# Performance work log

Hardware: AMD Instinct MI355X
Metric: run time of the kernel (lower is better)

## Reference

```python
import jax, jax.numpy as jnp
import numpy as np

NA, NKPT, NC = 3, 17, 1
NO_DET = NC + 5              # 6
NO = NO_DET + 3 * NKPT       # 57
ANCHORS = np.array([[19,27,44,40,38,94],[96,68,86,152,180,137],[140,301,303,264,238,542]], dtype=np.float32).reshape(3, 3, 2)
STRIDES = np.array([8.0, 16.0, 32.0], dtype=np.float32)
CH = (256, 512, 1024)
HW = (80, 40, 20)
B = 16


def setup_inputs():
    key = jax.random.key(0)
    ks = jax.random.split(key, 18)
    d = {}
    ki = 0
    for i, (c, hw) in enumerate(zip(CH, HW)):
        d[f"f{i}"] = jax.random.normal(ks[ki], (B, c, hw, hw), jnp.float32); ki += 1
        d[f"ia{i}"] = jax.random.normal(ks[ki], (1, c, 1, 1), jnp.float32) * 0.02; ki += 1
        d[f"w{i}"] = jax.random.normal(ks[ki], (NA * NO_DET, c), jnp.float32) * (1.0 / np.sqrt(c)); ki += 1
        d[f"b{i}"] = jnp.zeros((NA * NO_DET,), jnp.float32)
        d[f"im{i}"] = 1.0 + jax.random.normal(ks[ki], (1, NA * NO_DET, 1, 1), jnp.float32) * 0.02; ki += 1
        d[f"wk{i}"] = jax.random.normal(ks[ki], (NA * 3 * NKPT, c), jnp.float32) * (1.0 / np.sqrt(c)); ki += 1
        d[f"bk{i}"] = jnp.zeros((NA * 3 * NKPT,), jnp.float32)
    return d


def _decode(feat, ia, w, b, im, wk, bk, anchors_l, stride):
    # ImplicitA -> 1x1 conv -> ImplicitM (det branch); plain 1x1 conv (kpt branch)
    det = jnp.einsum('bchw,oc->bohw', feat + ia, w) + b[None, :, None, None]
    det = det * im
    kpt = jnp.einsum('bchw,oc->bohw', feat, wk) + bk[None, :, None, None]
    x = jnp.concatenate([det, kpt], axis=1)          # (B, na*no, H, W)
    Bb, _, H, W = x.shape
    x = x.reshape(Bb, NA, NO, H, W).transpose(0, 1, 3, 4, 2)  # (B, na, H, W, no)
    yv, xv = jnp.meshgrid(jnp.arange(H), jnp.arange(W), indexing='ij')
    grid = jnp.stack([xv, yv], -1).astype(x.dtype)[None, None]  # (1,1,H,W,2)
    xd = jax.nn.sigmoid(x[..., :NO_DET])
    xy = (xd[..., 0:2] * 2.0 - 0.5 + grid) * stride
    wh = (xd[..., 2:4] * 2.0) ** 2 * anchors_l.reshape(1, NA, 1, 1, 2)
    kp = x[..., NO_DET:]                              # (B, na, H, W, 51)
    kx = (kp[..., 0::3] * 2.0 - 0.5 + grid[..., 0:1]) * stride
    ky = (kp[..., 1::3] * 2.0 - 0.5 + grid[..., 1:2]) * stride
    kc = jax.nn.sigmoid(kp[..., 2::3])
    kdec = jnp.stack([kx, ky, kc], -1).reshape(Bb, NA, H, W, 3 * NKPT)
    y = jnp.concatenate([xy, wh, xd[..., 4:], kdec], -1)  # (B, na, H, W, 57)
    return y.reshape(Bb, -1, NO)


def reference(f0, ia0, w0, b0, im0, wk0, bk0,
              f1, ia1, w1, b1, im1, wk1, bk1,
              f2, ia2, w2, b2, im2, wk2, bk2):
    anchors = jnp.asarray(ANCHORS)
    z0 = _decode(f0, ia0, w0, b0, im0, wk0, bk0, anchors[0], STRIDES[0])
    z1 = _decode(f1, ia1, w1, b1, im1, wk1, bk1, anchors[1], STRIDES[1])
    z2 = _decode(f2, ia2, w2, b2, im2, wk2, bk2, anchors[2], STRIDES[2])
    return jnp.concatenate([z0, z1, z2], axis=1)      # (B, 25200, 57)
```

## Files before the change

### kernel.cpp

```cpp
#include <hip/hip_runtime.h>
#include <hip/hip_bf16.h>

typedef __attribute__((ext_vector_type(8))) short short8;
typedef __attribute__((ext_vector_type(4))) float floatx4;

__device__ __forceinline__ float sigm(float x) { return 1.0f / (1.0f + __expf(-x)); }

__device__ __forceinline__ unsigned short f2bf(float v) {
  union { __hip_bfloat16 h; unsigned short u; } cv;
  cv.h = __float2bfloat16(v);
  return cv.u;
}

__device__ __forceinline__ void glds16(const void* g, void* l) {
  __builtin_amdgcn_global_load_lds((const __attribute__((address_space(1))) void*)g,
                                   (__attribute__((address_space(3))) void*)l, 16, 0, 0);
}

struct PrepArgs {
  const float *w, *b, *im, *ia, *wk, *bk;
  unsigned short* Wp;
  float* bias;
  int C;
};

__global__ void prep_kernel(PrepArgs A0, PrepArgs A1, PrepArgs A2) {
  PrepArgs A = (blockIdx.y == 0) ? A0 : (blockIdx.y == 1) ? A1 : A2;
  const int n = blockIdx.x;
  const int t = threadIdx.x;
  const int C = A.C;
  unsigned short* wrow = A.Wp + (size_t)n * C;
  if (n >= 171) {
    for (int k = t; k < C; k += 64) wrow[k] = 0;
    if (t == 0) A.bias[n] = 0.0f;
    return;
  }
  if (n < 18) {
    const float* src = A.w + (size_t)n * C;
    const float sc = A.im[n];
    float dot = 0.0f;
    for (int k = t; k < C; k += 64) {
      float v = src[k];
      dot += v * A.ia[k];
      wrow[k] = f2bf(v * sc);
    }
#pragma unroll
    for (int off = 32; off > 0; off >>= 1) dot += __shfl_down(dot, off);
    if (t == 0) A.bias[n] = sc * (A.b[n] + dot);
  } else {
    const float* src = A.wk + (size_t)(n - 18) * C;
    for (int k = t; k < C; k += 64) wrow[k] = f2bf(src[k]);
    if (t == 0) A.bias[n] = A.bk[n - 18];
  }
}

#define LDS_BYTES 34560

template <int SC, int C, int HW, int W>
__device__ __forceinline__ void gemm_decode(const float* __restrict__ feat,
                                            const unsigned short* __restrict__ Wp,
                                            const float* __restrict__ bias,
                                            float* __restrict__ out, int tile, char* smem) {
  constexpr float STRD = (SC == 0) ? 8.0f : (SC == 1) ? 16.0f : 32.0f;
  constexpr int ZOFF = (SC == 0) ? 0 : (SC == 1) ? 19200 : 24000;
  constexpr int I = C / 64;

  const int t = threadIdx.x;
  const int lane = t & 63;
  const int wv = t >> 6;
  const int l15 = lane & 15;
  const int quad = lane >> 4;

  unsigned short* Alds = (unsigned short*)smem;
  char* BB = smem + 9216;
  float* Elds = (float*)smem;

  const int mA = tile * 64 + lane;
  const int bA = mA / HW;
  const int pA = mA - bA * HW;
  const float* fbase = feat + ((size_t)bA * C + wv * 16) * (size_t)HW + pA;

  const int rsub = lane >> 3;
  const int csw = (lane & 7) ^ rsub;
  const char* WpB = (const char*)Wp;

  floatx4 acc[11];
#pragma unroll
  for (int nj = 0; nj < 11; ++nj) acc[nj] = (floatx4){0.f, 0.f, 0.f, 0.f};

  const unsigned short* aRd = Alds + (wv * 16 + l15) * 72 + quad * 8;
  const int c0 = quad ^ (l15 & 7);
  const char* bRd0 = BB + (size_t)l15 * 128 + c0 * 16;
  const char* bRd1 = BB + (size_t)l15 * 128 + (c0 ^ 4) * 16;

  float v[16];
  auto loadA = [&](int it) {
    const float* g = fbase + (size_t)it * 64 * HW;
#pragma unroll
    for (int kk = 0; kk < 16; ++kk) v[kk] = g[(size_t)kk * HW];
  };
  auto writeA = [&]() {
    short8 s0, s1;
#pragma unroll
    for (int j = 0; j < 8; ++j) {
      s0[j] = (short)f2bf(v[j]);
      s1[j] = (short)f2bf(v[j + 8]);
    }
    *(short8*)(Alds + lane * 72 + wv * 16) = s0;
    *(short8*)(Alds + lane * 72 + wv * 16 + 8) = s1;
  };

  loadA(0);
  for (int it = 0; it < I; ++it) {
    asm volatile("s_barrier" ::: "memory");
#pragma unroll
    for (int j = 0; j < 6; ++j) {
      const int rowb = wv * 48 + j * 8;
      const void* gsrc = WpB + ((size_t)(rowb + rsub) * C + (size_t)it * 64) * 2 + csw * 16;
      glds16(gsrc, BB + rowb * 128);
    }
    __builtin_amdgcn_sched_barrier(0);
    writeA();
    loadA((it + 1 < I) ? it + 1 : it);
    __builtin_amdgcn_sched_barrier(0);
    asm volatile("s_waitcnt vmcnt(16) lgkmcnt(0)\n\ts_barrier" ::: "memory");
    short8 af0 = *(const short8*)(aRd);
    short8 af1 = *(const short8*)(aRd + 32);
#pragma unroll
    for (int nj = 0; nj < 11; ++nj) {
      short8 b0 = *(const short8*)(bRd0 + (size_t)nj * 2048);
      short8 b1 = *(const short8*)(bRd1 + (size_t)nj * 2048);
      acc[nj] = __builtin_amdgcn_mfma_f32_16x16x32_bf16(af0, b0, acc[nj], 0, 0, 0);
      acc[nj] = __builtin_amdgcn_mfma_f32_16x16x32_bf16(af1, b1, acc[nj], 0, 0, 0);
    }
  }

  float bj[11];
#pragma unroll
  for (int nj = 0; nj < 11; ++nj) bj[nj] = bias[nj * 16 + l15];

#pragma unroll
  for (int c = 0; c < 2; ++c) {
    __syncthreads();
    if ((wv >> 1) == c) {
      const int rbase = (wv & 1) * 16 + quad * 4;
#pragma unroll
      for (int nj = 0; nj < 11; ++nj)
#pragma unroll
        for (int r = 0; r < 4; ++r)
          Elds[(rbase + r) * 180 + nj * 16 + l15] = acc[nj][r] + bj[nj];
    }
    __syncthreads();
    if (t < 192) {
      const int task = t >> 1, half = t & 1;
      const int row = task & 31, a = task >> 5;
      const int m = tile * 64 + c * 32 + row;
      const int bb = m / HW;
      const int p = m - bb * HW;
      const float fx = (float)(p % W);
      const float fy = (float)(p / W);
      float* L = Elds + row * 180 + a * 57;
      if (half == 0) {
        float aw, ah;
        if constexpr (SC == 0) {
          aw = (a == 0) ? 19.f : (a == 1) ? 44.f : 38.f;
          ah = (a == 0) ? 27.f : (a == 1) ? 40.f : 94.f;
        } else if constexpr (SC == 1) {
          aw = (a == 0) ? 96.f : (a == 1) ? 86.f : 180.f;
          ah = (a == 0) ? 68.f : (a == 1) ? 152.f : 137.f;
        } else {
          aw = (a == 0) ? 140.f : (a == 1) ? 303.f : 238.f;
          ah = (a == 0) ? 301.f : (a == 1) ? 264.f : 542.f;
        }
        float r0 = L[0], r1 = L[1], r2 = L[2], r3 = L[3], r4 = L[4], r5 = L[5];
        L[0] = (sigm(r0) * 2.f - 0.5f + fx) * STRD;
        L[1] = (sigm(r1) * 2.f - 0.5f + fy) * STRD;
        float tw = sigm(r2) * 2.f;
        L[2] = tw * tw * aw;
        float th = sigm(r3) * 2.f;
        L[3] = th * th * ah;
        L[4] = sigm(r4);
        L[5] = sigm(r5);
#pragma unroll
        for (int kp = 0; kp < 8; ++kp) {
          float kx = L[6 + 3 * kp], ky = L[7 + 3 * kp], kc = L[8 + 3 * kp];
          L[6 + 3 * kp] = (kx * 2.f - 0.5f + fx) * STRD;
          L[7 + 3 * kp] = (ky * 2.f - 0.5f + fy) * STRD;
          L[8 + 3 * kp] = sigm(kc);
        }
      } else {
#pragma unroll
        for (int kp = 8; kp < 17; ++kp) {
          float kx = L[6 + 3 * kp], ky = L[7 + 3 * kp], kc = L[8 + 3 * kp];
          L[6 + 3 * kp] = (kx * 2.f - 0.5f + fx) * STRD;
          L[7 + 3 * kp] = (ky * 2.f - 0.5f + fy) * STRD;
          L[8 + 3 * kp] = sigm(kc);
        }
      }
    }
    __syncthreads();
    for (int i = t; i < 96 * 57; i += 256) {
      int sr = i / 57;
      int j = i - sr * 57;
      int a = sr >> 5, row = sr & 31;
      int m = tile * 64 + c * 32 + row;
      int bb = m / HW;
      int p = m - bb * HW;
      out[((size_t)bb * 25200 + (size_t)(ZOFF + a * HW + p)) * 57 + j] =
          Elds[row * 180 + a * 57 + j];
    }
  }
}

__global__ __launch_bounds__(256, 4) void main_kernel(
    const float* __restrict__ f0, const float* __restrict__ f1, const float* __restrict__ f2,
    const unsigned short* __restrict__ Wp0, const unsigned short* __restrict__ Wp1,
    const unsigned short* __restrict__ Wp2, const float* __restrict__ b0,
    const float* __restrict__ b1, const float* __restrict__ b2, float* __restrict__ out) {
  __shared__ __align__(16) char smem[LDS_BYTES];
  const int bid = blockIdx.x;
  if (bid < 100)
    gemm_decode<2, 1024, 400, 20>(f2, Wp2, b2, out, bid, smem);
  else if (bid < 500)
    gemm_decode<1, 512, 1600, 40>(f1, Wp1, b1, out, bid - 100, smem);
  else
    gemm_decode<0, 256, 6400, 80>(f0, Wp0, b0, out, bid - 500, smem);
}

extern "C" void kernel_launch(void* const* d_in, const int* in_sizes, int n_in, void* d_out,
                              int out_size, void* d_ws, size_t ws_size, hipStream_t stream) {
  const float *f[3], *ia[3], *w[3], *b[3], *im[3], *wk[3], *bk[3];
  for (int s = 0; s < 3; ++s) {
    f[s] = (const float*)d_in[7 * s + 0];
    ia[s] = (const float*)d_in[7 * s + 1];
    w[s] = (const float*)d_in[7 * s + 2];
    b[s] = (const float*)d_in[7 * s + 3];
    im[s] = (const float*)d_in[7 * s + 4];
    wk[s] = (const float*)d_in[7 * s + 5];
    bk[s] = (const float*)d_in[7 * s + 6];
  }
  char* ws = (char*)d_ws;
  unsigned short* Wp0 = (unsigned short*)(ws + 0);
  unsigned short* Wp1 = (unsigned short*)(ws + 98304);
  unsigned short* Wp2 = (unsigned short*)(ws + 294912);
  float* bias0 = (float*)(ws + 688128);
  float* bias1 = (float*)(ws + 688896);
  float* bias2 = (float*)(ws + 689664);

  PrepArgs A0 = {w[0], b[0], im[0], ia[0], wk[0], bk[0], Wp0, bias0, 256};
  PrepArgs A1 = {w[1], b[1], im[1], ia[1], wk[1], bk[1], Wp1, bias1, 512};
  PrepArgs A2 = {w[2], b[2], im[2], ia[2], wk[2], bk[2], Wp2, bias2, 1024};
  prep_kernel<<<dim3(192, 3), 64, 0, stream>>>(A0, A1, A2);

  main_kernel<<<2100, 256, 0, stream>>>(f[0], f[1], f[2], Wp0, Wp1, Wp2, bias0, bias1, bias2,
                                        (float*)d_out);
}
```

Before: 298.9 us.

## Load A fragments directly into registers and double-buffer weight tiles in LDS

Each lane now loads the A operand straight from global memory in the MFMA fragment layout, converts it to bf16 in registers, and no longer round-trips it through LDS. That removes the LDS write/read of A and one barrier per K-iteration. The weight (B) tile is double-buffered in LDS so the next iteration's global-to-LDS copy overlaps the current MFMAs. The cost is more LDS per block (48KB), so the launch bound drops from 4 to 3 blocks per CU, and the per-lane global loads on feat may be less coalesced.

Result: no change. 296.9 us (-0.6%).

```diff
diff --git a/kernel.cpp b/kernel.cpp
--- a/kernel.cpp
+++ b/kernel.cpp
@@ -54,7 +54,7 @@
   }
 }
 
-#define LDS_BYTES 34560
+#define LDS_BYTES 49152
 
 template <int SC, int C, int HW, int W>
 __device__ __forceinline__ void gemm_decode(const float* __restrict__ feat,
@@ -71,14 +71,13 @@
   const int l15 = lane & 15;
   const int quad = lane >> 4;
 
-  unsigned short* Alds = (unsigned short*)smem;
-  char* BB = smem + 9216;
+  char* BB = smem;
   float* Elds = (float*)smem;
 
-  const int mA = tile * 64 + lane;
+  const int mA = tile * 64 + wv * 16 + l15;
   const int bA = mA / HW;
   const int pA = mA - bA * HW;
-  const float* fbase = feat + ((size_t)bA * C + wv * 16) * (size_t)HW + pA;
+  const float* fbase = feat + ((size_t)bA * C + quad * 8) * (size_t)HW + pA;
 
   const int rsub = lane >> 3;
   const int csw = (lane & 7) ^ rsub;
@@ -88,48 +87,49 @@
 #pragma unroll
   for (int nj = 0; nj < 11; ++nj) acc[nj] = (floatx4){0.f, 0.f, 0.f, 0.f};
 
-  const unsigned short* aRd = Alds + (wv * 16 + l15) * 72 + quad * 8;
   const int c0 = quad ^ (l15 & 7);
-  const char* bRd0 = BB + (size_t)l15 * 128 + c0 * 16;
-  const char* bRd1 = BB + (size_t)l15 * 128 + (c0 ^ 4) * 16;
+  const int bOff0 = l15 * 128 + c0 * 16;
+  const int bOff1 = l15 * 128 + (c0 ^ 4) * 16;
 
   float v[16];
   auto loadA = [&](int it) {
     const float* g = fbase + (size_t)it * 64 * HW;
 #pragma unroll
-    for (int kk = 0; kk < 16; ++kk) v[kk] = g[(size_t)kk * HW];
+    for (int j = 0; j < 8; ++j) {
+      v[j] = g[(size_t)j * HW];
+      v[j + 8] = g[(size_t)(32 + j) * HW];
+    }
   };
-  auto writeA = [&]() {
-    short8 s0, s1;
-#pragma unroll
-    for (int j = 0; j < 8; ++j) {
-      s0[j] = (short)f2bf(v[j]);
-      s1[j] = (short)f2bf(v[j + 8]);
-    }
-    *(short8*)(Alds + lane * 72 + wv * 16) = s0;
-    *(short8*)(Alds + lane * 72 + wv * 16 + 8) = s1;
-  };
-
-  loadA(0);
-  for (int it = 0; it < I; ++it) {
-    asm volatile("s_barrier" ::: "memory");
+  auto stageB = [&](int it, int buf) {
 #pragma unroll
     for (int j = 0; j < 6; ++j) {
       const int rowb = wv * 48 + j * 8;
       const void* gsrc = WpB + ((size_t)(rowb + rsub) * C + (size_t)it * 64) * 2 + csw * 16;
-      glds16(gsrc, BB + rowb * 128);
-    }
+      glds16(gsrc, BB + buf * 24576 + rowb * 128);
+    }
+  };
+
+  stageB(0, 0);
+  loadA(0);
+
+  for (int it = 0; it < I; ++it) {
+    asm volatile("s_waitcnt vmcnt(16)\n\ts_barrier" ::: "memory");
+    stageB((it + 1 < I) ? it + 1 : 0, (it + 1) & 1);
     __builtin_amdgcn_sched_barrier(0);
-    writeA();
+    short8 af0, af1;
+#pragma unroll
+    for (int j = 0; j < 8; ++j) {
+      af0[j] = (short)f2bf(v[j]);
+      af1[j] = (short)f2bf(v[j + 8]);
+    }
+    __builtin_amdgcn_sched_barrier(0);
     loadA((it + 1 < I) ? it + 1 : it);
     __builtin_amdgcn_sched_barrier(0);
-    asm volatile("s_waitcnt vmcnt(16) lgkmcnt(0)\n\ts_barrier" ::: "memory");
-    short8 af0 = *(const short8*)(aRd);
-    short8 af1 = *(const short8*)(aRd + 32);
+    const char* bBase = BB + (it & 1) * 24576;
 #pragma unroll
     for (int nj = 0; nj < 11; ++nj) {
-      short8 b0 = *(const short8*)(bRd0 + (size_t)nj * 2048);
-      short8 b1 = *(const short8*)(bRd1 + (size_t)nj * 2048);
+      short8 b0 = *(const short8*)(bBase + bOff0 + (size_t)nj * 2048);
+      short8 b1 = *(const short8*)(bBase + bOff1 + (size_t)nj * 2048);
       acc[nj] = __builtin_amdgcn_mfma_f32_16x16x32_bf16(af0, b0, acc[nj], 0, 0, 0);
       acc[nj] = __builtin_amdgcn_mfma_f32_16x16x32_bf16(af1, b1, acc[nj], 0, 0, 0);
     }
@@ -212,7 +212,7 @@
   }
 }
 
-__global__ __launch_bounds__(256, 4) void main_kernel(
+__global__ __launch_bounds__(256, 3) void main_kernel(
     const float* __restrict__ f0, const float* __restrict__ f1, const float* __restrict__ f2,
     const unsigned short* __restrict__ Wp0, const unsigned short* __restrict__ Wp1,
     const unsigned short* __restrict__ Wp2, const float* __restrict__ b0,
```
